# Performance work log

Hardware: AMD Instinct MI355X
Metric: run time of the kernel (lower is better)

Reference implementation:

```python
import jax, jax.numpy as jnp
import numpy as np

N, E, H, G2, R = 50000, 800000, 64, 1024, 5  # nodes, edges, hidden, grid^2, rounds


def setup_inputs() -> dict:
    key = jax.random.key(0)
    ks = jax.random.split(key, 12)
    s = 0.05  # weight scale (xavier-ish)
    w = lambda k, shape: jax.random.normal(k, shape, jnp.float32) * s
    return dict(
        node_features=jax.random.normal(ks[0], (N, 2), jnp.float32),
        edge_attr=jax.random.normal(ks[1], (E, 4), jnp.float32),
        node_enc_W=w(ks[2], (2, H)), node_enc_b=jnp.zeros((H,), jnp.float32),
        edge_enc_W=w(ks[3], (4, H)), edge_enc_b=jnp.zeros((H,), jnp.float32),
        edge_mlp_W=w(ks[4], (R, 3 * H, H)), edge_mlp_b=jnp.zeros((R, H), jnp.float32),
        node_mlp_W=w(ks[5], (R, 2 * H, H)), node_mlp_b=jnp.zeros((R, H), jnp.float32),
        dec_W=w(ks[6], (H, H)), dec_b=jnp.zeros((H,), jnp.float32),
        hm1_W=w(ks[7], (H, H)), hm1_b=jnp.zeros((H,), jnp.float32),
        hm2_W=w(ks[8], (H, G2)), hm2_b=jnp.zeros((G2,), jnp.float32),
        edge_index=jax.random.randint(ks[9], (2, E), 0, N),
    )


def reference(node_features, edge_attr, node_enc_W, node_enc_b, edge_enc_W,
              edge_enc_b, edge_mlp_W, edge_mlp_b, node_mlp_W, node_mlp_b,
              dec_W, dec_b, hm1_W, hm1_b, hm2_W, hm2_b, edge_index):
    n_nodes = node_features.shape[0]
    src, dst = edge_index[0], edge_index[1]
    # encoders
    h = jax.nn.relu(node_features @ node_enc_W + node_enc_b)   # [N, H]
    e = jax.nn.relu(edge_attr @ edge_enc_W + edge_enc_b)       # [E, H]
    # message passing rounds (sum aggregation, mean_aggr=False)
    for r in range(edge_mlp_W.shape[0]):
        m_in = jnp.concatenate([h[src], h[dst], e], axis=-1)   # [E, 3H]
        m = jax.nn.relu(m_in @ edge_mlp_W[r] + edge_mlp_b[r])  # [E, H]
        aggr = jax.ops.segment_sum(m, dst, num_segments=n_nodes)  # [N, H]
        h = jax.nn.relu(jnp.concatenate([h, aggr], axis=-1) @ node_mlp_W[r] + node_mlp_b[r])
        e = m  # updated edge state carried to next round
    embeddings = h @ dec_W + dec_b                              # [N, H]
    logits = jax.nn.relu(embeddings @ hm1_W + hm1_b) @ hm2_W + hm2_b  # [N, G2]
    return embeddings, logits
```

## Files before the change

### kernel.cpp

```cpp
#include <hip/hip_runtime.h>

#define HD 64

typedef __attribute__((ext_vector_type(8))) short bf16x8;
typedef __attribute__((ext_vector_type(4))) float f32x4;

#define MFMA16(a, b, c) __builtin_amdgcn_mfma_f32_16x16x32_bf16(a, b, c, 0, 0, 0)

__device__ __forceinline__ float relu(float x) { return x > 0.f ? x : 0.f; }

__device__ __forceinline__ unsigned short f2bf(float f) {
  unsigned u = __float_as_uint(f);
  u += 0x7fff + ((u >> 16) & 1);
  return (unsigned short)(u >> 16);
}
__device__ __forceinline__ float bf2f(short s) {
  return __uint_as_float(((unsigned)(unsigned short)s) << 16);
}
__device__ __forceinline__ bf16x8 ldbf8(const unsigned short* p) {
  return *reinterpret_cast<const bf16x8*>(p);
}
__device__ __forceinline__ float4 ldf4(const float* p) {
  return *reinterpret_cast<const float4*>(p);
}

__global__ __launch_bounds__(256) void k_wt(const float* __restrict__ in,
                                            unsigned short* __restrict__ out,
                                            int K, int Nc) {
  int total = K * Nc;
  int idx = blockIdx.x * 256 + threadIdx.x;
  int b = blockIdx.y;
  if (idx >= total) return;
  int n = idx / K, k = idx - n * K;
  out[(size_t)b * total + idx] = f2bf(in[(size_t)b * total + (size_t)k * Nc + n]);
}

__global__ __launch_bounds__(256) void k_hist(const int* __restrict__ ei,
                                              int* __restrict__ deg, long long E_) {
  long long eid = (long long)blockIdx.x * 256 + threadIdx.x;
  if (eid >= E_) return;
  atomicAdd(deg + ei[E_ + eid], 1);
}

__global__ __launch_bounds__(1024) void k_scan(const int* __restrict__ deg,
                                               int* __restrict__ cnt, int N_) {
  __shared__ int s[1024];
  int t = threadIdx.x;
  int chunk = (N_ + 1023) / 1024;
  int lo = t * chunk, hi = lo + chunk;
  if (lo > N_) lo = N_;
  if (hi > N_) hi = N_;
  int sum = 0;
  for (int i = lo; i < hi; ++i) sum += deg[i];
  s[t] = sum;
  __syncthreads();
  for (int o = 1; o < 1024; o <<= 1) {
    int v = (t >= o) ? s[t - o] : 0;
    __syncthreads();
    s[t] += v;
    __syncthreads();
  }
  int base = (t == 0) ? 0 : s[t - 1];
  for (int i = lo; i < hi; ++i) {
    cnt[i] = base;
    base += deg[i];
  }
}

__global__ __launch_bounds__(256) void k_scatter(const int* __restrict__ ei,
                                                 int* __restrict__ cnt,
                                                 int* __restrict__ perm,
                                                 int* __restrict__ src_s,
                                                 int* __restrict__ dst_s, long long E_) {
  long long eid = (long long)blockIdx.x * 256 + threadIdx.x;
  if (eid >= E_) return;
  int s = ei[eid], d = ei[E_ + eid];
  int pos = atomicAdd(cnt + d, 1);
  perm[pos] = (int)eid;
  src_s[pos] = s;
  dst_s[pos] = d;
}

__global__ __launch_bounds__(256) void k_node_enc(
    const float* __restrict__ nf, const float* __restrict__ W,
    const float* __restrict__ b, unsigned short* __restrict__ h, int N_) {
  int t = blockIdx.x * 256 + threadIdx.x;
  int n = t >> 6, j = t & 63;
  if (n >= N_) return;
  float x0 = nf[(size_t)n * 2 + 0], x1 = nf[(size_t)n * 2 + 1];
  h[t] = f2bf(relu(fmaf(x0, W[j], fmaf(x1, W[HD + j], b[j]))));
}

__global__ __launch_bounds__(256) void k_pre(
    const unsigned short* __restrict__ h, const unsigned short* __restrict__ W12t,
    const float* __restrict__ be0, unsigned short* __restrict__ H12, int ntiles) {
  __shared__ float s[4][16][68];
  int wid = threadIdx.x >> 6, l = threadIdx.x & 63;
  int tile = blockIdx.x * 4 + wid;
  int lr = l & 15, lk = l >> 4;
  if (tile >= ntiles) return;
  int r0 = tile * 16;
  const unsigned short* hp = h + (size_t)(r0 + lr) * HD;
  f32x4 a1[4] = {}, a2[4] = {};
#pragma unroll
  for (int kk = 0; kk < 2; ++kk) {
    bf16x8 a = ldbf8(hp + kk * 32 + lk * 8);
#pragma unroll
    for (int nt = 0; nt < 4; ++nt) {
      bf16x8 b1 = ldbf8(W12t + (size_t)(nt * 16 + lr) * 64 + kk * 32 + lk * 8);
      bf16x8 b2 = ldbf8(W12t + 4096 + (size_t)(nt * 16 + lr) * 64 + kk * 32 + lk * 8);
      a1[nt] = MFMA16(a, b1, a1[nt]);
      a2[nt] = MFMA16(a, b2, a2[nt]);
    }
  }
  int erow = l >> 2, c0 = (l & 3) * 16;
#pragma unroll
  for (int nt = 0; nt < 4; ++nt) {
    float bias = be0[nt * 16 + lr];
#pragma unroll
    for (int i = 0; i < 4; ++i) s[wid][lk * 4 + i][nt * 16 + lr] = a1[nt][i] + bias;
  }
  {
    bf16x8 o0, o1;
#pragma unroll
    for (int j = 0; j < 8; ++j) {
      o0[j] = f2bf(s[wid][erow][c0 + j]);
      o1[j] = f2bf(s[wid][erow][c0 + 8 + j]);
    }
    unsigned short* op = H12 + (size_t)(r0 + erow) * 128 + c0;
    *reinterpret_cast<bf16x8*>(op) = o0;
    *reinterpret_cast<bf16x8*>(op + 8) = o1;
  }
#pragma unroll
  for (int nt = 0; nt < 4; ++nt)
#pragma unroll
    for (int i = 0; i < 4; ++i) s[wid][lk * 4 + i][nt * 16 + lr] = a2[nt][i];
  {
    bf16x8 o0, o1;
#pragma unroll
    for (int j = 0; j < 8; ++j) {
      o0[j] = f2bf(s[wid][erow][c0 + j]);
      o1[j] = f2bf(s[wid][erow][c0 + 8 + j]);
    }
    unsigned short* op = H12 + (size_t)(r0 + erow) * 128 + 64 + c0;
    *reinterpret_cast<bf16x8*>(op) = o0;
    *reinterpret_cast<bf16x8*>(op + 8) = o1;
  }
}

template <bool FUSE_ENC>
__global__ __launch_bounds__(256) void k_edge2(
    unsigned short* __restrict__ e, const unsigned short* __restrict__ H12,
    const int* __restrict__ src_s, const int* __restrict__ dst_s,
    const unsigned short* __restrict__ W3t,
    const float* __restrict__ ea, const int* __restrict__ perm,
    const float* __restrict__ We, const float* __restrict__ be) {
  __shared__ float smf[4][16][68];
  int wid = threadIdx.x >> 6, l = threadIdx.x & 63;
  int tile = blockIdx.x * 4 + wid;
  int r0 = tile * 16;
  int lr = l & 15, lk = l >> 4;
  int erow = l >> 2, c0 = (l & 3) * 16;

  int sidx = src_s[r0 + erow];
  int didx = dst_s[r0 + erow];
  const unsigned short* h1p = H12 + (size_t)sidx * 128 + c0;
  const unsigned short* h2p = H12 + (size_t)didx * 128 + 64 + c0;
  bf16x8 g1a = ldbf8(h1p), g1b = ldbf8(h1p + 8);
  bf16x8 g2a = ldbf8(h2p), g2b = ldbf8(h2p + 8);

  bf16x8 afrag[2];
  if (FUSE_ENC) {
    int eid = perm[r0 + lr];
    float4 row = ldf4(ea + (size_t)eid * 4);
#pragma unroll
    for (int kk = 0; kk < 2; ++kk) {
      int j0 = kk * 32 + lk * 8;
      float4 b0 = ldf4(be + j0), b1 = ldf4(be + j0 + 4);
      float v[8] = {b0.x, b0.y, b0.z, b0.w, b1.x, b1.y, b1.z, b1.w};
#pragma unroll
      for (int c = 0; c < 4; ++c) {
        float x = (c == 0) ? row.x : (c == 1) ? row.y : (c == 2) ? row.z : row.w;
        float4 w0 = ldf4(We + c * 64 + j0), w1 = ldf4(We + c * 64 + j0 + 4);
        v[0] = fmaf(x, w0.x, v[0]); v[1] = fmaf(x, w0.y, v[1]);
        v[2] = fmaf(x, w0.z, v[2]); v[3] = fmaf(x, w0.w, v[3]);
        v[4] = fmaf(x, w1.x, v[4]); v[5] = fmaf(x, w1.y, v[5]);
        v[6] = fmaf(x, w1.z, v[6]); v[7] = fmaf(x, w1.w, v[7]);
      }
#pragma unroll
      for (int q = 0; q < 8; ++q) afrag[kk][q] = (short)f2bf(relu(v[q]));
    }
  } else {
    const unsigned short* ep = e + (size_t)(r0 + lr) * HD;
    afrag[0] = ldbf8(ep + lk * 8);
    afrag[1] = ldbf8(ep + 32 + lk * 8);
  }

  f32x4 acc[4] = {};
#pragma unroll
  for (int kk = 0; kk < 2; ++kk) {
#pragma unroll
    for (int nt = 0; nt < 4; ++nt) {
      bf16x8 bb = ldbf8(W3t + (size_t)(nt * 16 + lr) * 64 + kk * 32 + lk * 8);
      acc[nt] = MFMA16(afrag[kk], bb, acc[nt]);
    }
  }
#pragma unroll
  for (int nt = 0; nt < 4; ++nt)
#pragma unroll
    for (int i = 0; i < 4; ++i)
      smf[wid][lk * 4 + i][nt * 16 + lr] = acc[nt][i];

  float g1f[16], g2f[16];
#pragma unroll
  for (int j = 0; j < 8; ++j) {
    g1f[j] = bf2f(g1a[j]); g1f[8 + j] = bf2f(g1b[j]);
    g2f[j] = bf2f(g2a[j]); g2f[8 + j] = bf2f(g2b[j]);
  }
  bf16x8 o0, o1;
#pragma unroll
  for (int q = 0; q < 4; ++q) {
    float4 s4 = ldf4(&smf[wid][erow][c0 + q * 4]);
    float v0 = relu(s4.x + g1f[q * 4 + 0] + g2f[q * 4 + 0]);
    float v1 = relu(s4.y + g1f[q * 4 + 1] + g2f[q * 4 + 1]);
    float v2 = relu(s4.z + g1f[q * 4 + 2] + g2f[q * 4 + 2]);
    float v3 = relu(s4.w + g1f[q * 4 + 3] + g2f[q * 4 + 3]);
    if (q < 2) {
      o0[q * 4 + 0] = f2bf(v0); o0[q * 4 + 1] = f2bf(v1);
      o0[q * 4 + 2] = f2bf(v2); o0[q * 4 + 3] = f2bf(v3);
    } else {
      o1[(q - 2) * 4 + 0] = f2bf(v0); o1[(q - 2) * 4 + 1] = f2bf(v1);
      o1[(q - 2) * 4 + 2] = f2bf(v2); o1[(q - 2) * 4 + 3] = f2bf(v3);
    }
  }
  size_t eb = ((size_t)r0 + erow) * HD + c0;
  *reinterpret_cast<bf16x8*>(&e[eb]) = o0;
  *reinterpret_cast<bf16x8*>(&e[eb + 8]) = o1;
}

__global__ __launch_bounds__(256) void k_node_csr(
    unsigned short* __restrict__ h, const unsigned short* __restrict__ m,
    const int* __restrict__ cnt,
    const unsigned short* __restrict__ Wt, const float* __restrict__ b,
    const unsigned short* __restrict__ W12t,
    const float* __restrict__ be_next,
    unsigned short* __restrict__ H12, int ntiles) {
  __shared__ float smf[4][16][68];
  int wid = threadIdx.x >> 6, l = threadIdx.x & 63;
  int tile = blockIdx.x * 4 + wid;
  if (tile >= ntiles) return;
  int r0 = tile * 16;
  int lr = l & 15, lk = l >> 4;

  int node = r0 + lr;
  int q16 = lk * 16;
  int beg = (node == 0) ? 0 : cnt[node - 1];
  int end = cnt[node];
  float s0[16];
#pragma unroll
  for (int j = 0; j < 16; ++j) s0[j] = 0.f;
  for (int i = beg; i < end; ++i) {
    const unsigned short* mp = m + (size_t)i * HD + q16;
    bf16x8 v0 = ldbf8(mp);
    bf16x8 v1 = ldbf8(mp + 8);
#pragma unroll
    for (int j = 0; j < 8; ++j) {
      s0[j] += bf2f(v0[j]);
      s0[8 + j] += bf2f(v1[j]);
    }
  }
#pragma unroll
  for (int j = 0; j < 16; ++j) smf[wid][lr][q16 + j] = s0[j];

  bf16x8 aagg[2];
#pragma unroll
  for (int kk = 0; kk < 2; ++kk) {
    const float* sp = &smf[wid][lr][kk * 32 + lk * 8];
    float4 f0 = ldf4(sp), f1 = ldf4(sp + 4);
    aagg[kk][0] = f2bf(f0.x); aagg[kk][1] = f2bf(f0.y);
    aagg[kk][2] = f2bf(f0.z); aagg[kk][3] = f2bf(f0.w);
    aagg[kk][4] = f2bf(f1.x); aagg[kk][5] = f2bf(f1.y);
    aagg[kk][6] = f2bf(f1.z); aagg[kk][7] = f2bf(f1.w);
  }

  f32x4 acc[4] = {};
#pragma unroll
  for (int kk = 0; kk < 4; ++kk) {
    bf16x8 a = (kk < 2) ? ldbf8(h + (size_t)(r0 + lr) * HD + kk * 32 + lk * 8)
                        : aagg[kk - 2];
#pragma unroll
    for (int nt = 0; nt < 4; ++nt) {
      bf16x8 bb = ldbf8(Wt + (size_t)(kk >> 1) * 4096 +
                        (size_t)(nt * 16 + lr) * 64 + (kk & 1) * 32 + lk * 8);
      acc[nt] = MFMA16(a, bb, acc[nt]);
    }
  }

#pragma unroll
  for (int nt = 0; nt < 4; ++nt) {
    float bias = b[nt * 16 + lr];
#pragma unroll
    for (int i = 0; i < 4; ++i)
      smf[wid][lk * 4 + i][nt * 16 + lr] = relu(acc[nt][i] + bias);
  }
  int erow = l >> 2, c0 = (l & 3) * 16;
  {
    bf16x8 o0, o1;
#pragma unroll
    for (int j = 0; j < 8; ++j) {
      o0[j] = f2bf(smf[wid][erow][c0 + j]);
      o1[j] = f2bf(smf[wid][erow][c0 + 8 + j]);
    }
    size_t hb = ((size_t)r0 + erow) * HD + c0;
    *reinterpret_cast<bf16x8*>(&h[hb]) = o0;
    *reinterpret_cast<bf16x8*>(&h[hb + 8]) = o1;
  }

  if (!W12t) return;

  bf16x8 ah[2];
#pragma unroll
  for (int kk = 0; kk < 2; ++kk) {
    const float* sp = &smf[wid][lr][kk * 32 + lk * 8];
    float4 f0 = ldf4(sp), f1 = ldf4(sp + 4);
    ah[kk][0] = f2bf(f0.x); ah[kk][1] = f2bf(f0.y);
    ah[kk][2] = f2bf(f0.z); ah[kk][3] = f2bf(f0.w);
    ah[kk][4] = f2bf(f1.x); ah[kk][5] = f2bf(f1.y);
    ah[kk][6] = f2bf(f1.z); ah[kk][7] = f2bf(f1.w);
  }
  f32x4 a1[4] = {}, a2[4] = {};
#pragma unroll
  for (int kk = 0; kk < 2; ++kk) {
#pragma unroll
    for (int nt = 0; nt < 4; ++nt) {
      bf16x8 b1 = ldbf8(W12t + (size_t)(nt * 16 + lr) * 64 + kk * 32 + lk * 8);
      bf16x8 b2 = ldbf8(W12t + 4096 + (size_t)(nt * 16 + lr) * 64 + kk * 32 + lk * 8);
      a1[nt] = MFMA16(ah[kk], b1, a1[nt]);
      a2[nt] = MFMA16(ah[kk], b2, a2[nt]);
    }
  }
#pragma unroll
  for (int nt = 0; nt < 4; ++nt) {
    float bias = be_next[nt * 16 + lr];
#pragma unroll
    for (int i = 0; i < 4; ++i)
      smf[wid][lk * 4 + i][nt * 16 + lr] = a1[nt][i] + bias;
  }
  {
    bf16x8 o0, o1;
#pragma unroll
    for (int j = 0; j < 8; ++j) {
      o0[j] = f2bf(smf[wid][erow][c0 + j]);
      o1[j] = f2bf(smf[wid][erow][c0 + 8 + j]);
    }
    unsigned short* op = H12 + (size_t)(r0 + erow) * 128 + c0;
    *reinterpret_cast<bf16x8*>(op) = o0;
    *reinterpret_cast<bf16x8*>(op + 8) = o1;
  }
#pragma unroll
  for (int nt = 0; nt < 4; ++nt)
#pragma unroll
    for (int i = 0; i < 4; ++i)
      smf[wid][lk * 4 + i][nt * 16 + lr] = a2[nt][i];
  {
    bf16x8 o0, o1;
#pragma unroll
    for (int j = 0; j < 8; ++j) {
      o0[j] = f2bf(smf[wid][erow][c0 + j]);
      o1[j] = f2bf(smf[wid][erow][c0 + 8 + j]);
    }
    unsigned short* op = H12 + (size_t)(r0 + erow) * 128 + 64 + c0;
    *reinterpret_cast<bf16x8*>(op) = o0;
    *reinterpret_cast<bf16x8*>(op + 8) = o1;
  }
}

__global__ __launch_bounds__(256) void k_gemm64(
    const unsigned short* __restrict__ Ab, const float* __restrict__ Af,
    const unsigned short* __restrict__ Wt, const float* __restrict__ b,
    float* __restrict__ outf, unsigned short* __restrict__ outb,
    int do_relu, int ntiles) {
  int wid = threadIdx.x >> 6, l = threadIdx.x & 63;
  int tile = blockIdx.x * 4 + wid;
  if (tile >= ntiles) return;
  int r0 = tile * 16;
  int lr = l & 15, lk = l >> 4;

  f32x4 acc[4] = {};
#pragma unroll
  for (int kk = 0; kk < 2; ++kk) {
    bf16x8 a;
    int off = kk * 32 + lk * 8;
    if (Af) {
      const float* ap = Af + (size_t)(r0 + lr) * HD + off;
      float4 f0 = ldf4(ap);
      float4 f1 = ldf4(ap + 4);
      a[0] = f2bf(f0.x); a[1] = f2bf(f0.y); a[2] = f2bf(f0.z); a[3] = f2bf(f0.w);
      a[4] = f2bf(f1.x); a[5] = f2bf(f1.y); a[6] = f2bf(f1.z); a[7] = f2bf(f1.w);
    } else {
      a = ldbf8(Ab + (size_t)(r0 + lr) * HD + off);
    }
#pragma unroll
    for (int nt = 0; nt < 4; ++nt) {
      bf16x8 bb = ldbf8(Wt + (size_t)(nt * 16 + lr) * HD + off);
      acc[nt] = MFMA16(a, bb, acc[nt]);
    }
  }
#pragma unroll
  for (int nt = 0; nt < 4; ++nt) {
    int col = nt * 16 + lr;
    float bias = b[col];
#pragma unroll
    for (int i = 0; i < 4; ++i) {
      float v = acc[nt][i] + bias;
      if (do_relu) v = relu(v);
      size_t o = (size_t)(r0 + lk * 4 + i) * HD + col;
      if (outf) outf[o] = v;
      if (outb) outb[o] = f2bf(v);
    }
  }
}

__global__ __launch_bounds__(256) void k_head_mfma(
    const unsigned short* __restrict__ A, const unsigned short* __restrict__ Wt,
    const float* __restrict__ b2, float* __restrict__ out) {
  __shared__ float sf[4][16][68];
  int wid = threadIdx.x >> 6, l = threadIdx.x & 63;
  int task = blockIdx.x * 4 + wid;
  int mt = task >> 4, ng = task & 15;
  int r0 = mt * 16, n0 = ng * 64;
  int lr = l & 15, lk = l >> 4;

  f32x4 acc[4] = {};
#pragma unroll
  for (int kk = 0; kk < 2; ++kk) {
    bf16x8 a = ldbf8(A + (size_t)(r0 + lr) * HD + kk * 32 + lk * 8);
#pragma unroll
    for (int nt = 0; nt < 4; ++nt) {
      bf16x8 bb = ldbf8(Wt + (size_t)(n0 + nt * 16 + lr) * HD + kk * 32 + lk * 8);
      acc[nt] = MFMA16(a, bb, acc[nt]);
    }
  }
#pragma unroll
  for (int nt = 0; nt < 4; ++nt) {
    int col = nt * 16 + lr;
    float bias = b2[n0 + col];
#pragma unroll
    for (int i = 0; i < 4; ++i) sf[wid][lk * 4 + i][col] = acc[nt][i] + bias;
  }
  int row = l >> 2, cb = (l & 3) * 16;
  float* op = out + (size_t)(r0 + row) * 1024 + n0 + cb;
#pragma unroll
  for (int q = 0; q < 4; ++q)
    *reinterpret_cast<float4*>(op + q * 4) = ldf4(&sf[wid][row][cb + q * 4]);
}

extern "C" void kernel_launch(void* const* d_in, const int* in_sizes, int n_in,
                              void* d_out, int out_size, void* d_ws, size_t ws_size,
                              hipStream_t stream) {
  const float* node_features = (const float*)d_in[0];
  const float* edge_attr     = (const float*)d_in[1];
  const float* node_enc_W    = (const float*)d_in[2];
  const float* node_enc_b    = (const float*)d_in[3];
  const float* edge_enc_W    = (const float*)d_in[4];
  const float* edge_enc_b    = (const float*)d_in[5];
  const float* edge_mlp_W    = (const float*)d_in[6];
  const float* edge_mlp_b    = (const float*)d_in[7];
  const float* node_mlp_W    = (const float*)d_in[8];
  const float* node_mlp_b    = (const float*)d_in[9];
  const float* dec_W         = (const float*)d_in[10];
  const float* dec_b         = (const float*)d_in[11];
  const float* hm1_W         = (const float*)d_in[12];
  const float* hm1_b         = (const float*)d_in[13];
  const float* hm2_W         = (const float*)d_in[14];
  const float* hm2_b         = (const float*)d_in[15];
  const int*   edge_index    = (const int*)d_in[16];

  const int N_ = in_sizes[0] / 2;
  const long long E_ = in_sizes[1] / 4;
  const int R_ = in_sizes[7] / HD;

  char* p = (char*)d_ws;
  unsigned short* e_bf = (unsigned short*)p; p += (size_t)E_ * HD * 2;
  unsigned short* h_bf = (unsigned short*)p; p += (size_t)N_ * HD * 2;
  unsigned short* H12  = (unsigned short*)p; p += (size_t)N_ * 128 * 2;
  unsigned short* t_bf = (unsigned short*)p; p += (size_t)N_ * HD * 2;
  unsigned short* wt_edge = (unsigned short*)p; p += (size_t)R_ * 3 * 64 * 64 * 2;
  unsigned short* wt_node = (unsigned short*)p; p += (size_t)R_ * 2 * 64 * 64 * 2;
  unsigned short* wt_dec = (unsigned short*)p;  p += 64 * 64 * 2;
  unsigned short* wt_hm1 = (unsigned short*)p;  p += 64 * 64 * 2;
  unsigned short* wt_hm2 = (unsigned short*)p;  p += 1024 * 64 * 2;
  int* perm  = (int*)p; p += (size_t)E_ * 4;
  int* src_s = (int*)p; p += (size_t)E_ * 4;
  int* dst_s = (int*)p; p += (size_t)E_ * 4;
  int* deg   = (int*)p; p += (size_t)N_ * 4;
  int* cnt   = (int*)p; p += (size_t)N_ * 4;

  k_wt<<<dim3((64 * 64 + 255) / 256, 3 * R_), 256, 0, stream>>>(edge_mlp_W, wt_edge, 64, 64);
  k_wt<<<dim3((64 * 64 + 255) / 256, 2 * R_), 256, 0, stream>>>(node_mlp_W, wt_node, 64, 64);
  k_wt<<<dim3((64 * 64 + 255) / 256, 1), 256, 0, stream>>>(dec_W, wt_dec, 64, 64);
  k_wt<<<dim3((64 * 64 + 255) / 256, 1), 256, 0, stream>>>(hm1_W, wt_hm1, 64, 64);
  k_wt<<<dim3((64 * 1024 + 255) / 256, 1), 256, 0, stream>>>(hm2_W, wt_hm2, 64, 1024);

  const int e_blocks = (int)((E_ + 255) / 256);
  hipMemsetAsync(deg, 0, (size_t)N_ * 4, stream);
  k_hist<<<e_blocks, 256, 0, stream>>>(edge_index, deg, E_);
  k_scan<<<1, 1024, 0, stream>>>(deg, cnt, N_);
  k_scatter<<<e_blocks, 256, 0, stream>>>(edge_index, cnt, perm, src_s, dst_s, E_);

  const int nh_blocks = (int)(((size_t)N_ * HD + 255) / 256);
  k_node_enc<<<nh_blocks, 256, 0, stream>>>(node_features, node_enc_W, node_enc_b, h_bf, N_);

  const int etile_blocks = (int)(E_ / 64);
  const int ntiles = (N_ + 15) / 16;
  const int nblocks = (ntiles + 3) / 4;

  k_pre<<<nblocks, 256, 0, stream>>>(h_bf, wt_edge, edge_mlp_b, H12, ntiles);

  for (int r = 0; r < R_; ++r) {
    const unsigned short* W3t = wt_edge + (size_t)r * 3 * 4096 + 2 * 4096;
    if (r == 0) {
      k_edge2<true><<<etile_blocks, 256, 0, stream>>>(
          e_bf, H12, src_s, dst_s, W3t, edge_attr, perm, edge_enc_W, edge_enc_b);
    } else {
      k_edge2<false><<<etile_blocks, 256, 0, stream>>>(
          e_bf, H12, src_s, dst_s, W3t, nullptr, nullptr, nullptr, nullptr);
    }
    const unsigned short* w12_next =
        (r + 1 < R_) ? (wt_edge + (size_t)(r + 1) * 3 * 4096) : nullptr;
    const float* be_next = edge_mlp_b + (size_t)(r + 1 < R_ ? r + 1 : 0) * HD;
    k_node_csr<<<nblocks, 256, 0, stream>>>(
        h_bf, e_bf, cnt, wt_node + (size_t)r * 2 * 4096,
        node_mlp_b + (size_t)r * HD, w12_next, be_next, H12, ntiles);
  }

  float* out_emb = (float*)d_out;
  float* out_log = out_emb + (size_t)N_ * HD;
  k_gemm64<<<nblocks, 256, 0, stream>>>(h_bf, nullptr, wt_dec, dec_b, out_emb, nullptr, 0, ntiles);
  k_gemm64<<<nblocks, 256, 0, stream>>>(nullptr, out_emb, wt_hm1, hm1_b, nullptr, t_bf, 1, ntiles);
  k_head_mfma<<<ntiles * 4, 256, 0, stream>>>(t_bf, wt_hm2, hm2_b, out_log);
}
```

Measured before the change: 877.7 us.

## Fuse edge MLP and node aggregation/update into one per-round node-tiled kernel

Replaces the separate per-round edge kernel and CSR node kernel with a single kernel. Each wave owns 16 destination nodes, computes messages for their dst-sorted incoming edges, and reduces them into LDS segment sums. The node MLP and the next round's H12 projection then run in the same kernel, using ping-pong H12 buffers to avoid read/write races across tiles. This removes the round-trip of messages through global memory for aggregation and skips writing edge state in the last round. In exchange, edge work is now load-imbalanced across node tiles by degree, and the aggregation walks edges serially per 16-edge chunk.

```diff
diff --git a/kernel.cpp b/kernel.cpp
--- a/kernel.cpp
+++ b/kernel.cpp
@@ -94,7 +94,7 @@
 __global__ __launch_bounds__(256) void k_pre(
     const unsigned short* __restrict__ h, const unsigned short* __restrict__ W12t,
     const float* __restrict__ be0, unsigned short* __restrict__ H12, int ntiles) {
-  __shared__ float s[4][16][68];
+  __shared__ __align__(16) float s[4][16][68];
   int wid = threadIdx.x >> 6, l = threadIdx.x & 63;
   int tile = blockIdx.x * 4 + wid;
   int lr = l & 15, lk = l >> 4;
@@ -148,180 +148,195 @@
   }
 }
 
-template <bool FUSE_ENC>
-__global__ __launch_bounds__(256) void k_edge2(
-    unsigned short* __restrict__ e, const unsigned short* __restrict__ H12,
-    const int* __restrict__ src_s, const int* __restrict__ dst_s,
+template <bool FUSE_ENC, bool LAST>
+__global__ __launch_bounds__(256) void k_round(
+    unsigned short* __restrict__ h, unsigned short* __restrict__ e,
+    const unsigned short* __restrict__ H12in, unsigned short* __restrict__ H12out,
+    const int* __restrict__ cnt, const int* __restrict__ src_s,
+    const int* __restrict__ dst_s,
     const unsigned short* __restrict__ W3t,
+    const unsigned short* __restrict__ Wn,
+    const float* __restrict__ bn,
+    const unsigned short* __restrict__ W12n,
+    const float* __restrict__ be_next,
     const float* __restrict__ ea, const int* __restrict__ perm,
-    const float* __restrict__ We, const float* __restrict__ be) {
-  __shared__ float smf[4][16][68];
-  int wid = threadIdx.x >> 6, l = threadIdx.x & 63;
-  int tile = blockIdx.x * 4 + wid;
-  int r0 = tile * 16;
-  int lr = l & 15, lk = l >> 4;
-  int erow = l >> 2, c0 = (l & 3) * 16;
-
-  int sidx = src_s[r0 + erow];
-  int didx = dst_s[r0 + erow];
-  const unsigned short* h1p = H12 + (size_t)sidx * 128 + c0;
-  const unsigned short* h2p = H12 + (size_t)didx * 128 + 64 + c0;
-  bf16x8 g1a = ldbf8(h1p), g1b = ldbf8(h1p + 8);
-  bf16x8 g2a = ldbf8(h2p), g2b = ldbf8(h2p + 8);
-
-  bf16x8 afrag[2];
-  if (FUSE_ENC) {
-    int eid = perm[r0 + lr];
-    float4 row = ldf4(ea + (size_t)eid * 4);
-#pragma unroll
-    for (int kk = 0; kk < 2; ++kk) {
-      int j0 = kk * 32 + lk * 8;
-      float4 b0 = ldf4(be + j0), b1 = ldf4(be + j0 + 4);
-      float v[8] = {b0.x, b0.y, b0.z, b0.w, b1.x, b1.y, b1.z, b1.w};
-#pragma unroll
-      for (int c = 0; c < 4; ++c) {
-        float x = (c == 0) ? row.x : (c == 1) ? row.y : (c == 2) ? row.z : row.w;
-        float4 w0 = ldf4(We + c * 64 + j0), w1 = ldf4(We + c * 64 + j0 + 4);
-        v[0] = fmaf(x, w0.x, v[0]); v[1] = fmaf(x, w0.y, v[1]);
-        v[2] = fmaf(x, w0.z, v[2]); v[3] = fmaf(x, w0.w, v[3]);
-        v[4] = fmaf(x, w1.x, v[4]); v[5] = fmaf(x, w1.y, v[5]);
-        v[6] = fmaf(x, w1.z, v[6]); v[7] = fmaf(x, w1.w, v[7]);
-      }
-#pragma unroll
-      for (int q = 0; q < 8; ++q) afrag[kk][q] = (short)f2bf(relu(v[q]));
-    }
-  } else {
-    const unsigned short* ep = e + (size_t)(r0 + lr) * HD;
-    afrag[0] = ldbf8(ep + lk * 8);
-    afrag[1] = ldbf8(ep + 32 + lk * 8);
-  }
-
-  f32x4 acc[4] = {};
-#pragma unroll
-  for (int kk = 0; kk < 2; ++kk) {
-#pragma unroll
-    for (int nt = 0; nt < 4; ++nt) {
-      bf16x8 bb = ldbf8(W3t + (size_t)(nt * 16 + lr) * 64 + kk * 32 + lk * 8);
-      acc[nt] = MFMA16(afrag[kk], bb, acc[nt]);
-    }
-  }
-#pragma unroll
-  for (int nt = 0; nt < 4; ++nt)
-#pragma unroll
-    for (int i = 0; i < 4; ++i)
-      smf[wid][lk * 4 + i][nt * 16 + lr] = acc[nt][i];
-
-  float g1f[16], g2f[16];
-#pragma unroll
-  for (int j = 0; j < 8; ++j) {
-    g1f[j] = bf2f(g1a[j]); g1f[8 + j] = bf2f(g1b[j]);
-    g2f[j] = bf2f(g2a[j]); g2f[8 + j] = bf2f(g2b[j]);
-  }
-  bf16x8 o0, o1;
-#pragma unroll
-  for (int q = 0; q < 4; ++q) {
-    float4 s4 = ldf4(&smf[wid][erow][c0 + q * 4]);
-    float v0 = relu(s4.x + g1f[q * 4 + 0] + g2f[q * 4 + 0]);
-    float v1 = relu(s4.y + g1f[q * 4 + 1] + g2f[q * 4 + 1]);
-    float v2 = relu(s4.z + g1f[q * 4 + 2] + g2f[q * 4 + 2]);
-    float v3 = relu(s4.w + g1f[q * 4 + 3] + g2f[q * 4 + 3]);
-    if (q < 2) {
-      o0[q * 4 + 0] = f2bf(v0); o0[q * 4 + 1] = f2bf(v1);
-      o0[q * 4 + 2] = f2bf(v2); o0[q * 4 + 3] = f2bf(v3);
-    } else {
-      o1[(q - 2) * 4 + 0] = f2bf(v0); o1[(q - 2) * 4 + 1] = f2bf(v1);
-      o1[(q - 2) * 4 + 2] = f2bf(v2); o1[(q - 2) * 4 + 3] = f2bf(v3);
-    }
-  }
-  size_t eb = ((size_t)r0 + erow) * HD + c0;
-  *reinterpret_cast<bf16x8*>(&e[eb]) = o0;
-  *reinterpret_cast<bf16x8*>(&e[eb + 8]) = o1;
-}
-
-__global__ __launch_bounds__(256) void k_node_csr(
-    unsigned short* __restrict__ h, const unsigned short* __restrict__ m,
-    const int* __restrict__ cnt,
-    const unsigned short* __restrict__ Wt, const float* __restrict__ b,
-    const unsigned short* __restrict__ W12t,
-    const float* __restrict__ be_next,
-    unsigned short* __restrict__ H12, int ntiles) {
-  __shared__ float smf[4][16][68];
+    const float* __restrict__ We, const float* __restrict__ be,
+    int ntiles, int E_) {
+  __shared__ __align__(16) float m_lds[4][16][68];
+  __shared__ __align__(16) float aggr_lds[4][16][68];
+  __shared__ __align__(16) float h2_lds[4][16][68];
   int wid = threadIdx.x >> 6, l = threadIdx.x & 63;
   int tile = blockIdx.x * 4 + wid;
   if (tile >= ntiles) return;
-  int r0 = tile * 16;
+  int base = tile * 16;
   int lr = l & 15, lk = l >> 4;
-
-  int node = r0 + lr;
-  int q16 = lk * 16;
-  int beg = (node == 0) ? 0 : cnt[node - 1];
-  int end = cnt[node];
-  float s0[16];
-#pragma unroll
-  for (int j = 0; j < 16; ++j) s0[j] = 0.f;
-  for (int i = beg; i < end; ++i) {
-    const unsigned short* mp = m + (size_t)i * HD + q16;
-    bf16x8 v0 = ldbf8(mp);
-    bf16x8 v1 = ldbf8(mp + 8);
-#pragma unroll
-    for (int j = 0; j < 8; ++j) {
-      s0[j] += bf2f(v0[j]);
-      s0[8 + j] += bf2f(v1[j]);
-    }
-  }
-#pragma unroll
-  for (int j = 0; j < 16; ++j) smf[wid][lr][q16 + j] = s0[j];
+  int erow = l >> 2, c0 = (l & 3) * 16;
+
+  {
+    const unsigned short* hp = H12in + (size_t)(base + erow) * 128 + 64 + c0;
+    bf16x8 v0 = ldbf8(hp), v1 = ldbf8(hp + 8);
+#pragma unroll
+    for (int j = 0; j < 8; ++j) {
+      h2_lds[wid][erow][c0 + j] = bf2f(v0[j]);
+      h2_lds[wid][erow][c0 + 8 + j] = bf2f(v1[j]);
+    }
+  }
+#pragma unroll
+  for (int j = 0; j < 16; ++j) aggr_lds[wid][lr][lk * 16 + j] = 0.f;
+
+  int beg = (base == 0) ? 0 : cnt[base - 1];
+  int end = cnt[base + 15];
+
+  float sum = 0.f;
+  int prev = (beg < end) ? dst_s[beg] : base;
+
+  for (int t = beg; t < end; t += 16) {
+    int i2 = t + erow;
+    bool valid = i2 < end;
+    int i2c = min(i2, E_ - 1);
+    int sidx = src_s[i2c];
+    int di = valid ? (dst_s[i2c] - base) : 0;
+    const unsigned short* h1p = H12in + (size_t)sidx * 128 + c0;
+    bf16x8 g1a = ldbf8(h1p), g1b = ldbf8(h1p + 8);
+
+    int ia = min(t + lr, E_ - 1);
+    bf16x8 afrag[2];
+    if (FUSE_ENC) {
+      int eid = perm[ia];
+      float4 row = ldf4(ea + (size_t)eid * 4);
+#pragma unroll
+      for (int kk = 0; kk < 2; ++kk) {
+        int j0 = kk * 32 + lk * 8;
+        float4 b0 = ldf4(be + j0), b1 = ldf4(be + j0 + 4);
+        float v[8] = {b0.x, b0.y, b0.z, b0.w, b1.x, b1.y, b1.z, b1.w};
+#pragma unroll
+        for (int c = 0; c < 4; ++c) {
+          float x = (c == 0) ? row.x : (c == 1) ? row.y : (c == 2) ? row.z : row.w;
+          float4 w0 = ldf4(We + c * 64 + j0), w1 = ldf4(We + c * 64 + j0 + 4);
+          v[0] = fmaf(x, w0.x, v[0]); v[1] = fmaf(x, w0.y, v[1]);
+          v[2] = fmaf(x, w0.z, v[2]); v[3] = fmaf(x, w0.w, v[3]);
+          v[4] = fmaf(x, w1.x, v[4]); v[5] = fmaf(x, w1.y, v[5]);
+          v[6] = fmaf(x, w1.z, v[6]); v[7] = fmaf(x, w1.w, v[7]);
+        }
+#pragma unroll
+        for (int q = 0; q < 8; ++q) afrag[kk][q] = (short)f2bf(relu(v[q]));
+      }
+    } else {
+      const unsigned short* ep = e + (size_t)ia * HD;
+      afrag[0] = ldbf8(ep + lk * 8);
+      afrag[1] = ldbf8(ep + 32 + lk * 8);
+    }
+
+    f32x4 acc[4] = {};
+#pragma unroll
+    for (int kk = 0; kk < 2; ++kk) {
+#pragma unroll
+      for (int nt = 0; nt < 4; ++nt) {
+        bf16x8 bb = ldbf8(W3t + (size_t)(nt * 16 + lr) * 64 + kk * 32 + lk * 8);
+        acc[nt] = MFMA16(afrag[kk], bb, acc[nt]);
+      }
+    }
+#pragma unroll
+    for (int nt = 0; nt < 4; ++nt)
+#pragma unroll
+      for (int i = 0; i < 4; ++i)
+        m_lds[wid][lk * 4 + i][nt * 16 + lr] = acc[nt][i];
+
+    float g1f[16];
+#pragma unroll
+    for (int j = 0; j < 8; ++j) {
+      g1f[j] = bf2f(g1a[j]);
+      g1f[8 + j] = bf2f(g1b[j]);
+    }
+    float v[16];
+#pragma unroll
+    for (int q = 0; q < 4; ++q) {
+      float4 s4 = ldf4(&m_lds[wid][erow][c0 + q * 4]);
+      float4 h2 = ldf4(&h2_lds[wid][di][c0 + q * 4]);
+      v[q * 4 + 0] = relu(s4.x + g1f[q * 4 + 0] + h2.x);
+      v[q * 4 + 1] = relu(s4.y + g1f[q * 4 + 1] + h2.y);
+      v[q * 4 + 2] = relu(s4.z + g1f[q * 4 + 2] + h2.z);
+      v[q * 4 + 3] = relu(s4.w + g1f[q * 4 + 3] + h2.w);
+    }
+    if (!LAST && valid) {
+      bf16x8 o0, o1;
+#pragma unroll
+      for (int j = 0; j < 8; ++j) {
+        o0[j] = f2bf(v[j]);
+        o1[j] = f2bf(v[8 + j]);
+      }
+      size_t eb = (size_t)i2 * HD + c0;
+      *reinterpret_cast<bf16x8*>(&e[eb]) = o0;
+      *reinterpret_cast<bf16x8*>(&e[eb + 8]) = o1;
+    }
+#pragma unroll
+    for (int q = 0; q < 4; ++q) {
+      float4 s4 = make_float4(v[q * 4], v[q * 4 + 1], v[q * 4 + 2], v[q * 4 + 3]);
+      *reinterpret_cast<float4*>(&m_lds[wid][erow][c0 + q * 4]) = s4;
+    }
+
+#pragma unroll
+    for (int r = 0; r < 16; ++r) {
+      int i = t + r;
+      if (i >= end) break;
+      int dc = dst_s[i];
+      if (dc != prev) {
+        aggr_lds[wid][prev - base][l] = sum;
+        sum = 0.f;
+        prev = dc;
+      }
+      sum += m_lds[wid][r][l];
+    }
+  }
+  if (beg < end) aggr_lds[wid][prev - base][l] = sum;
 
   bf16x8 aagg[2];
 #pragma unroll
   for (int kk = 0; kk < 2; ++kk) {
-    const float* sp = &smf[wid][lr][kk * 32 + lk * 8];
+    const float* sp = &aggr_lds[wid][lr][kk * 32 + lk * 8];
     float4 f0 = ldf4(sp), f1 = ldf4(sp + 4);
     aagg[kk][0] = f2bf(f0.x); aagg[kk][1] = f2bf(f0.y);
     aagg[kk][2] = f2bf(f0.z); aagg[kk][3] = f2bf(f0.w);
     aagg[kk][4] = f2bf(f1.x); aagg[kk][5] = f2bf(f1.y);
     aagg[kk][6] = f2bf(f1.z); aagg[kk][7] = f2bf(f1.w);
   }
-
   f32x4 acc[4] = {};
 #pragma unroll
   for (int kk = 0; kk < 4; ++kk) {
-    bf16x8 a = (kk < 2) ? ldbf8(h + (size_t)(r0 + lr) * HD + kk * 32 + lk * 8)
+    bf16x8 a = (kk < 2) ? ldbf8(h + (size_t)(base + lr) * HD + kk * 32 + lk * 8)
                         : aagg[kk - 2];
 #pragma unroll
     for (int nt = 0; nt < 4; ++nt) {
-      bf16x8 bb = ldbf8(Wt + (size_t)(kk >> 1) * 4096 +
+      bf16x8 bb = ldbf8(Wn + (size_t)(kk >> 1) * 4096 +
                         (size_t)(nt * 16 + lr) * 64 + (kk & 1) * 32 + lk * 8);
       acc[nt] = MFMA16(a, bb, acc[nt]);
     }
   }
-
 #pragma unroll
   for (int nt = 0; nt < 4; ++nt) {
-    float bias = b[nt * 16 + lr];
+    float bias = bn[nt * 16 + lr];
 #pragma unroll
     for (int i = 0; i < 4; ++i)
-      smf[wid][lk * 4 + i][nt * 16 + lr] = relu(acc[nt][i] + bias);
-  }
-  int erow = l >> 2, c0 = (l & 3) * 16;
+      m_lds[wid][lk * 4 + i][nt * 16 + lr] = relu(acc[nt][i] + bias);
+  }
   {
     bf16x8 o0, o1;
 #pragma unroll
     for (int j = 0; j < 8; ++j) {
-      o0[j] = f2bf(smf[wid][erow][c0 + j]);
-      o1[j] = f2bf(smf[wid][erow][c0 + 8 + j]);
-    }
-    size_t hb = ((size_t)r0 + erow) * HD + c0;
+      o0[j] = f2bf(m_lds[wid][erow][c0 + j]);
+      o1[j] = f2bf(m_lds[wid][erow][c0 + 8 + j]);
+    }
+    size_t hb = (size_t)(base + erow) * HD + c0;
     *reinterpret_cast<bf16x8*>(&h[hb]) = o0;
     *reinterpret_cast<bf16x8*>(&h[hb + 8]) = o1;
   }
 
-  if (!W12t) return;
+  if (LAST) return;
 
   bf16x8 ah[2];
 #pragma unroll
   for (int kk = 0; kk < 2; ++kk) {
-    const float* sp = &smf[wid][lr][kk * 32 + lk * 8];
+    const float* sp = &m_lds[wid][lr][kk * 32 + lk * 8];
     float4 f0 = ldf4(sp), f1 = ldf4(sp + 4);
     ah[kk][0] = f2bf(f0.x); ah[kk][1] = f2bf(f0.y);
     ah[kk][2] = f2bf(f0.z); ah[kk][3] = f2bf(f0.w);
@@ -333,8 +348,8 @@
   for (int kk = 0; kk < 2; ++kk) {
 #pragma unroll
     for (int nt = 0; nt < 4; ++nt) {
-      bf16x8 b1 = ldbf8(W12t + (size_t)(nt * 16 + lr) * 64 + kk * 32 + lk * 8);
-      bf16x8 b2 = ldbf8(W12t + 4096 + (size_t)(nt * 16 + lr) * 64 + kk * 32 + lk * 8);
+      bf16x8 b1 = ldbf8(W12n + (size_t)(nt * 16 + lr) * 64 + kk * 32 + lk * 8);
+      bf16x8 b2 = ldbf8(W12n + 4096 + (size_t)(nt * 16 + lr) * 64 + kk * 32 + lk * 8);
       a1[nt] = MFMA16(ah[kk], b1, a1[nt]);
       a2[nt] = MFMA16(ah[kk], b2, a2[nt]);
     }
@@ -344,16 +359,16 @@
     float bias = be_next[nt * 16 + lr];
 #pragma unroll
     for (int i = 0; i < 4; ++i)
-      smf[wid][lk * 4 + i][nt * 16 + lr] = a1[nt][i] + bias;
+      m_lds[wid][lk * 4 + i][nt * 16 + lr] = a1[nt][i] + bias;
   }
   {
     bf16x8 o0, o1;
 #pragma unroll
     for (int j = 0; j < 8; ++j) {
-      o0[j] = f2bf(smf[wid][erow][c0 + j]);
-      o1[j] = f2bf(smf[wid][erow][c0 + 8 + j]);
-    }
-    unsigned short* op = H12 + (size_t)(r0 + erow) * 128 + c0;
+      o0[j] = f2bf(m_lds[wid][erow][c0 + j]);
+      o1[j] = f2bf(m_lds[wid][erow][c0 + 8 + j]);
+    }
+    unsigned short* op = H12out + (size_t)(base + erow) * 128 + c0;
     *reinterpret_cast<bf16x8*>(op) = o0;
     *reinterpret_cast<bf16x8*>(op + 8) = o1;
   }
@@ -361,15 +376,15 @@
   for (int nt = 0; nt < 4; ++nt)
 #pragma unroll
     for (int i = 0; i < 4; ++i)
-      smf[wid][lk * 4 + i][nt * 16 + lr] = a2[nt][i];
+      m_lds[wid][lk * 4 + i][nt * 16 + lr] = a2[nt][i];
   {
     bf16x8 o0, o1;
 #pragma unroll
     for (int j = 0; j < 8; ++j) {
-      o0[j] = f2bf(smf[wid][erow][c0 + j]);
-      o1[j] = f2bf(smf[wid][erow][c0 + 8 + j]);
-    }
-    unsigned short* op = H12 + (size_t)(r0 + erow) * 128 + 64 + c0;
+      o0[j] = f2bf(m_lds[wid][erow][c0 + j]);
+      o1[j] = f2bf(m_lds[wid][erow][c0 + 8 + j]);
+    }
+    unsigned short* op = H12out + (size_t)(base + erow) * 128 + 64 + c0;
     *reinterpret_cast<bf16x8*>(op) = o0;
     *reinterpret_cast<bf16x8*>(op + 8) = o1;
   }
@@ -424,7 +439,7 @@
 __global__ __launch_bounds__(256) void k_head_mfma(
     const unsigned short* __restrict__ A, const unsigned short* __restrict__ Wt,
     const float* __restrict__ b2, float* __restrict__ out) {
-  __shared__ float sf[4][16][68];
+  __shared__ __align__(16) float sf[4][16][68];
   int wid = threadIdx.x >> 6, l = threadIdx.x & 63;
   int task = blockIdx.x * 4 + wid;
   int mt = task >> 4, ng = task & 15;
@@ -483,7 +498,8 @@
   char* p = (char*)d_ws;
   unsigned short* e_bf = (unsigned short*)p; p += (size_t)E_ * HD * 2;
   unsigned short* h_bf = (unsigned short*)p; p += (size_t)N_ * HD * 2;
-  unsigned short* H12  = (unsigned short*)p; p += (size_t)N_ * 128 * 2;
+  unsigned short* H12a = (unsigned short*)p; p += (size_t)N_ * 128 * 2;
+  unsigned short* H12b = (unsigned short*)p; p += (size_t)N_ * 128 * 2;
   unsigned short* t_bf = (unsigned short*)p; p += (size_t)N_ * HD * 2;
   unsigned short* wt_edge = (unsigned short*)p; p += (size_t)R_ * 3 * 64 * 64 * 2;
   unsigned short* wt_node = (unsigned short*)p; p += (size_t)R_ * 2 * 64 * 64 * 2;
@@ -511,27 +527,38 @@
   const int nh_blocks = (int)(((size_t)N_ * HD + 255) / 256);
   k_node_enc<<<nh_blocks, 256, 0, stream>>>(node_features, node_enc_W, node_enc_b, h_bf, N_);
 
-  const int etile_blocks = (int)(E_ / 64);
   const int ntiles = (N_ + 15) / 16;
   const int nblocks = (ntiles + 3) / 4;
 
-  k_pre<<<nblocks, 256, 0, stream>>>(h_bf, wt_edge, edge_mlp_b, H12, ntiles);
-
+  k_pre<<<nblocks, 256, 0, stream>>>(h_bf, wt_edge, edge_mlp_b, H12a, ntiles);
+
+  unsigned short* bufs[2] = {H12a, H12b};
   for (int r = 0; r < R_; ++r) {
     const unsigned short* W3t = wt_edge + (size_t)r * 3 * 4096 + 2 * 4096;
-    if (r == 0) {
-      k_edge2<true><<<etile_blocks, 256, 0, stream>>>(
-          e_bf, H12, src_s, dst_s, W3t, edge_attr, perm, edge_enc_W, edge_enc_b);
-    } else {
-      k_edge2<false><<<etile_blocks, 256, 0, stream>>>(
-          e_bf, H12, src_s, dst_s, W3t, nullptr, nullptr, nullptr, nullptr);
-    }
-    const unsigned short* w12_next =
-        (r + 1 < R_) ? (wt_edge + (size_t)(r + 1) * 3 * 4096) : nullptr;
+    const unsigned short* Wn = wt_node + (size_t)r * 2 * 4096;
+    const float* bn = node_mlp_b + (size_t)r * HD;
+    const unsigned short* W12n =
+        (r + 1 < R_) ? (wt_edge + (size_t)(r + 1) * 3 * 4096) : wt_edge;
     const float* be_next = edge_mlp_b + (size_t)(r + 1 < R_ ? r + 1 : 0) * HD;
-    k_node_csr<<<nblocks, 256, 0, stream>>>(
-        h_bf, e_bf, cnt, wt_node + (size_t)r * 2 * 4096,
-        node_mlp_b + (size_t)r * HD, w12_next, be_next, H12, ntiles);
+    const unsigned short* H12in = bufs[r & 1];
+    unsigned short* H12out = bufs[(r + 1) & 1];
+    bool fuse = (r == 0), last = (r == R_ - 1);
+    if (fuse && !last)
+      k_round<true, false><<<nblocks, 256, 0, stream>>>(
+          h_bf, e_bf, H12in, H12out, cnt, src_s, dst_s, W3t, Wn, bn, W12n, be_next,
+          edge_attr, perm, edge_enc_W, edge_enc_b, ntiles, (int)E_);
+    else if (!fuse && !last)
+      k_round<false, false><<<nblocks, 256, 0, stream>>>(
+          h_bf, e_bf, H12in, H12out, cnt, src_s, dst_s, W3t, Wn, bn, W12n, be_next,
+          nullptr, nullptr, nullptr, nullptr, ntiles, (int)E_);
+    else if (!fuse && last)
+      k_round<false, true><<<nblocks, 256, 0, stream>>>(
+          h_bf, e_bf, H12in, H12out, cnt, src_s, dst_s, W3t, Wn, bn, W12n, be_next,
+          nullptr, nullptr, nullptr, nullptr, ntiles, (int)E_);
+    else
+      k_round<true, true><<<nblocks, 256, 0, stream>>>(
+          h_bf, e_bf, H12in, H12out, cnt, src_s, dst_s, W3t, Wn, bn, W12n, be_next,
+          edge_attr, perm, edge_enc_W, edge_enc_b, ntiles, (int)E_);
   }
 
   float* out_emb = (float*)d_out;
```

Measured after the change: 1.213 ms. +38.2%, slower.
